# Kernel tuning notes

Hardware: AMD Instinct MI355X
Metric: run time of the kernel (lower is better)

The kernel has to match this reference:

```python
import jax, jax.numpy as jnp
import numpy as np

N = 100_000   # nodes
E = 1_600_000 # edges (avg degree 16)
D = 64        # node feature / conv width
L = 3         # num conv layers
M = 128       # final mlp hidden
BN_EPS = 1e-5


def setup_inputs() -> dict:
    key = jax.random.key(0)
    ks = jax.random.split(key, 12)
    s = np.float32(1.0 / np.sqrt(D))
    sm = np.float32(1.0 / np.sqrt(M))
    return dict(
        x=jax.random.normal(ks[0], (N, D), jnp.float32),
        edge_src=jax.random.randint(ks[1], (E,), 0, N, dtype=jnp.int32),
        edge_dst=jax.random.randint(ks[2], (E,), 0, N, dtype=jnp.int32),
        W1=jax.random.normal(ks[3], (L, D, D), jnp.float32) * s,
        b1=jnp.zeros((L, D), jnp.float32),
        g1=jnp.ones((L, D), jnp.float32),
        be1=jnp.zeros((L, D), jnp.float32),
        W2=jax.random.normal(ks[4], (L, D, D), jnp.float32) * s,
        b2=jnp.zeros((L, D), jnp.float32),
        eps_gin=jnp.zeros((L,), jnp.float32),  # train_eps=True, init 0
        g_bn=jnp.ones((L, D), jnp.float32),
        b_bn=jnp.zeros((L, D), jnp.float32),
        Wf1=jax.random.normal(ks[5], (D, M), jnp.float32) * s,
        bf1=jnp.zeros((M,), jnp.float32),
        gf=jnp.ones((M,), jnp.float32),
        bef=jnp.zeros((M,), jnp.float32),
        Wf2=jax.random.normal(ks[6], (M, 1), jnp.float32) * sm,
        bf2=jnp.zeros((1,), jnp.float32),
    )


def _bn(h, g, b):
    # BatchNorm1d training-mode forward over node dim (biased variance)
    m = h.mean(axis=0)
    v = h.var(axis=0)
    return (h - m) * jax.lax.rsqrt(v + BN_EPS) * g + b


def reference(x, edge_src, edge_dst, W1, b1, g1, be1, W2, b2, eps_gin,
              g_bn, b_bn, Wf1, bf1, gf, bef, Wf2, bf2):
    for i in range(L):
        # GIN aggregation: sum of neighbor features (scatter-add over edges)
        agg = jax.ops.segment_sum(x[edge_src], edge_dst, num_segments=N)
        h = (1.0 + eps_gin[i]) * x + agg
        # GIN nn: Linear -> BatchNorm -> LeakyReLU -> Linear
        h = h @ W1[i] + b1[i]
        h = jax.nn.leaky_relu(_bn(h, g1[i], be1[i]))  # slope 0.01 = torch default
        x = h @ W2[i] + b2[i]
        # outer BatchNorm + activation on all but last conv layer
        if i != L - 1:
            x = jax.nn.leaky_relu(_bn(x, g_bn[i], b_bn[i]))
    # final head: Linear -> BN -> LeakyReLU -> Linear(->1), flatten
    h = x @ Wf1 + bf1
    h = jax.nn.leaky_relu(_bn(h, gf, bef))
    out = h @ Wf2 + bf2
    return out.ravel()  # [N]
```

## Files before the change

kernel.cpp:

```cpp
#include <hip/hip_runtime.h>

#define LRELU(x) ((x) > 0.0f ? (x) : 0.01f * (x))
#define UAF __uint_as_float
#define NSLOT 16

#if defined(__has_builtin)
#if __has_builtin(__builtin_amdgcn_fdot2_f32_bf16)
#define HAS_DOT2BF 1
#endif
#endif
#ifndef HAS_DOT2BF
#define HAS_DOT2BF 0
#endif

__device__ inline uint pack_bf16_rne(float x, float y) {
    uint lo = __float_as_uint(x);
    uint hi = __float_as_uint(y);
    lo = (lo + 0x7fffu + ((lo >> 16) & 1u)) >> 16;
    hi = (hi + 0x7fffu + ((hi >> 16) & 1u)) & 0xffff0000u;
    return lo | hi;
}

__device__ inline float dot2bf(uint a, uint b, float c) {
#if HAS_DOT2BF
    typedef __bf16 bf16x2 __attribute__((ext_vector_type(2)));
    return __builtin_amdgcn_fdot2_f32_bf16(__builtin_bit_cast(bf16x2, a),
                                           __builtin_bit_cast(bf16x2, b), c, false);
#else
    c += UAF(a << 16) * UAF(b << 16);
    c += UAF(a & 0xffff0000u) * UAF(b & 0xffff0000u);
    return c;
#endif
}

__global__ void zero_kernel(float* p, int n) {
    int i = blockIdx.x * blockDim.x + threadIdx.x;
    if (i < n) p[i] = 0.0f;
}

__global__ __launch_bounds__(256) void bhist_kernel(const int* __restrict__ dst,
                                                    int* __restrict__ bcnt, int E, int NB) {
    __shared__ int h[512];
    for (int i = threadIdx.x; i < NB; i += 256) h[i] = 0;
    __syncthreads();
    int base = blockIdx.x * 8192;
    int end = min(E, base + 8192);
    for (int e = base + threadIdx.x; e < end; e += 256) atomicAdd(&h[dst[e] >> 8], 1);
    __syncthreads();
    for (int i = threadIdx.x; i < NB; i += 256)
        if (h[i]) atomicAdd(&bcnt[i], h[i]);
}

__global__ __launch_bounds__(512) void bscan_kernel(const int* __restrict__ bcnt,
                                                    int* __restrict__ boff,
                                                    int* __restrict__ bcur, int NB) {
    __shared__ int sh[512];
    int t = threadIdx.x;
    int v = (t < NB) ? bcnt[t] : 0;
    sh[t] = v;
    __syncthreads();
    for (int o = 1; o < 512; o <<= 1) {
        int u = (t >= o) ? sh[t - o] : 0;
        __syncthreads();
        sh[t] += u;
        __syncthreads();
    }
    if (t < NB) {
        boff[t] = sh[t] - v;
        bcur[t] = sh[t] - v;
    }
}

__global__ __launch_bounds__(256) void bscatter_kernel(const int* __restrict__ src,
                                                       const int* __restrict__ dst,
                                                       int* __restrict__ bcur,
                                                       uint* __restrict__ pairs, int E, int NB) {
    __shared__ int h[512];
    __shared__ int bbase[512];
    for (int i = threadIdx.x; i < NB; i += 256) h[i] = 0;
    __syncthreads();
    int base = blockIdx.x * 8192;
    int end = min(E, base + 8192);
    for (int e = base + threadIdx.x; e < end; e += 256) atomicAdd(&h[dst[e] >> 8], 1);
    __syncthreads();
    for (int i = threadIdx.x; i < NB; i += 256) {
        bbase[i] = h[i] ? atomicAdd(&bcur[i], h[i]) : 0;
        h[i] = 0;
    }
    __syncthreads();
    for (int e = base + threadIdx.x; e < end; e += 256) {
        int d = dst[e];
        int b = d >> 8;
        int o = atomicAdd(&h[b], 1);
        pairs[bbase[b] + o] = ((uint)src[e] << 8) | (uint)(d & 255);
    }
}

__global__ __launch_bounds__(256) void bcsr_kernel(const uint* __restrict__ pairs,
                                                   const int* __restrict__ boff,
                                                   int* __restrict__ ptr, int* __restrict__ cnt,
                                                   int* __restrict__ nbr, int N, int NB, int E) {
    __shared__ int h[256];
    __shared__ int sc[256];
    int b = blockIdx.x;
    int lo = boff[b];
    int hi = (b + 1 < NB) ? boff[b + 1] : E;
    int t = threadIdx.x;
    h[t] = 0;
    __syncthreads();
    for (int i = lo + t; i < hi; i += 256) atomicAdd(&h[pairs[i] & 255u], 1);
    __syncthreads();
    int v = h[t];
    sc[t] = v;
    __syncthreads();
    for (int o = 1; o < 256; o <<= 1) {
        int u = (t >= o) ? sc[t - o] : 0;
        __syncthreads();
        sc[t] += u;
        __syncthreads();
    }
    int excl = sc[t] - v;
    int node = (b << 8) + t;
    if (node < N) {
        ptr[node] = lo + excl;
        cnt[node] = v;
    }
    __syncthreads();
    h[t] = excl;
    __syncthreads();
    for (int i = lo + t; i < hi; i += 256) {
        uint p = pairs[i];
        int ld = p & 255u;
        int o = atomicAdd(&h[ld], 1);
        nbr[lo + o] = (int)(p >> 8);
    }
}

__global__ void packw_kernel(const float* __restrict__ W1, const float* __restrict__ W2,
                             uint* __restrict__ Wp) {
    int id = blockIdx.x * blockDim.x + threadIdx.x;
    if (id >= 6 * 2048) return;
    int mat = id >> 11;
    int r = id & 2047;
    int kp = r >> 6, c = r & 63;
    const float* Ws = (mat < 3) ? (W1 + (size_t)mat * 4096) : (W2 + (size_t)(mat - 3) * 4096);
    Wp[id] = pack_bf16_rne(Ws[(size_t)(2 * kp) * 64 + c], Ws[(size_t)(2 * kp + 1) * 64 + c]);
}

__global__ __launch_bounds__(256) void to_bf16_kernel(const float* __restrict__ in,
                                                      uint* __restrict__ table, int n8) {
    int i = blockIdx.x * blockDim.x + threadIdx.x;
    if (i >= n8) return;
    float4 a = *(const float4*)&in[(size_t)i * 8];
    float4 b = *(const float4*)&in[(size_t)i * 8 + 4];
    uint4 p = make_uint4(pack_bf16_rne(a.x, a.y), pack_bf16_rne(a.z, a.w),
                         pack_bf16_rne(b.x, b.y), pack_bf16_rne(b.z, b.w));
    *(uint4*)&table[(size_t)i * 4] = p;
}

__global__ void finalize_kernel(const float* __restrict__ sums, const float* __restrict__ g,
                                const float* __restrict__ be, float* __restrict__ scale,
                                float* __restrict__ shift, int C, float invN) {
    int d = threadIdx.x;
    if (d >= C) return;
    float s = 0.0f, s2 = 0.0f;
    for (int k = 0; k < NSLOT; k++) {
        s += sums[k * 2 * C + d];
        s2 += sums[k * 2 * C + C + d];
    }
    float mean = s * invN;
    float var = s2 * invN - mean * mean;
    float sc = g[d] * rsqrtf(var + 1e-5f);
    scale[d] = sc;
    shift[d] = be[d] - mean * sc;
}

template <bool ACT>
__global__ __launch_bounds__(256) void gather_kernel(
    const uint* __restrict__ tb, const int* __restrict__ ptr, const int* __restrict__ cnt,
    const int* __restrict__ nbr, const float* __restrict__ eps_gin, int layer,
    const float* __restrict__ scale, const float* __restrict__ shift, uint* __restrict__ agg,
    int N) {
    int gtid = blockIdx.x * blockDim.x + threadIdx.x;
    int node = gtid >> 6;
    if (node >= N) return;
    int lane = threadIdx.x & 63;
    int half = lane >> 5;
    int sl = lane & 31;
    float sc0 = 1.0f, sh0 = 0.0f, sc1 = 1.0f, sh1 = 0.0f;
    if (ACT) {
        sc0 = scale[2 * sl + 0];
        sh0 = shift[2 * sl + 0];
        sc1 = scale[2 * sl + 1];
        sh1 = shift[2 * sl + 1];
    }
    int start = ptr[node];
    int deg = cnt[node];
    float a0 = 0.0f, a1 = 0.0f;
    int j = half;
    for (; j + 14 < deg; j += 16) {
        int ni[8];
        uint vv[8];
#pragma unroll
        for (int q = 0; q < 8; q++) ni[q] = nbr[start + j + 2 * q];
#pragma unroll
        for (int q = 0; q < 8; q++) vv[q] = tb[(size_t)ni[q] * 32 + sl];
#pragma unroll
        for (int q = 0; q < 8; q++) {
            float f0 = UAF(vv[q] << 16), f1 = UAF(vv[q] & 0xffff0000u);
            if (ACT) {
                f0 = LRELU(f0 * sc0 + sh0);
                f1 = LRELU(f1 * sc1 + sh1);
            }
            a0 += f0;
            a1 += f1;
        }
    }
    for (; j + 6 < deg; j += 8) {
        int ni[4];
        uint vv[4];
#pragma unroll
        for (int q = 0; q < 4; q++) ni[q] = nbr[start + j + 2 * q];
#pragma unroll
        for (int q = 0; q < 4; q++) vv[q] = tb[(size_t)ni[q] * 32 + sl];
#pragma unroll
        for (int q = 0; q < 4; q++) {
            float f0 = UAF(vv[q] << 16), f1 = UAF(vv[q] & 0xffff0000u);
            if (ACT) {
                f0 = LRELU(f0 * sc0 + sh0);
                f1 = LRELU(f1 * sc1 + sh1);
            }
            a0 += f0;
            a1 += f1;
        }
    }
    for (; j < deg; j += 2) {
        uint vA = tb[(size_t)nbr[start + j] * 32 + sl];
        float f0 = UAF(vA << 16), f1 = UAF(vA & 0xffff0000u);
        if (ACT) {
            f0 = LRELU(f0 * sc0 + sh0);
            f1 = LRELU(f1 * sc1 + sh1);
        }
        a0 += f0;
        a1 += f1;
    }
    a0 += __shfl(a0, lane ^ 32);
    a1 += __shfl(a1, lane ^ 32);
    uint vs = tb[(size_t)node * 32 + sl];
    float s0 = UAF(vs << 16), s1 = UAF(vs & 0xffff0000u);
    if (ACT) {
        s0 = LRELU(s0 * sc0 + sh0);
        s1 = LRELU(s1 * sc1 + sh1);
    }
    float ep = 1.0f + eps_gin[layer];
    a0 += ep * s0;
    a1 += ep * s1;
    if (half == 0) agg[(size_t)node * 32 + sl] = pack_bf16_rne(a0, a1);
}

template <bool INBN, bool OUTB, int MINW>
__global__ __launch_bounds__(256, MINW) void gemm_bf16_kernel(
    const uint* __restrict__ inb, const float* __restrict__ inf, const uint* __restrict__ Wp,
    const float* __restrict__ bias, const float* __restrict__ scale,
    const float* __restrict__ shift, uint* __restrict__ outb, float* __restrict__ outf,
    float* __restrict__ sums, int nrows) {
    constexpr int COLS = 64;
    __shared__ uint smem[32 * 68 + 32 * COLS];
    uint* inT = smem;
    uint* wsb = smem + 32 * 68;
    int t = threadIdx.x;
    int row0 = blockIdx.x * 64;

    if (!INBN) {
        for (int i = 0; i < 2; i++) {
            int f = t + 256 * i;
            int r = f >> 3, q = f & 7;
            int gr = row0 + r;
            uint4 v = make_uint4(0, 0, 0, 0);
            if (gr < nrows) v = *(const uint4*)&inb[(size_t)gr * 32 + q * 4];
            inT[(4 * q + 0) * 68 + r] = v.x;
            inT[(4 * q + 1) * 68 + r] = v.y;
            inT[(4 * q + 2) * 68 + r] = v.z;
            inT[(4 * q + 3) * 68 + r] = v.w;
        }
    } else {
        for (int i = 0; i < 4; i++) {
            int f = t + 256 * i;
            int r = f >> 4, q = f & 15;
            int gr = row0 + r;
            float4 v = make_float4(0.f, 0.f, 0.f, 0.f);
            if (gr < nrows) v = *(const float4*)&inf[(size_t)gr * 64 + q * 4];
            int d = 4 * q;
            float e0 = LRELU(v.x * scale[d + 0] + shift[d + 0]);
            float e1 = LRELU(v.y * scale[d + 1] + shift[d + 1]);
            float e2 = LRELU(v.z * scale[d + 2] + shift[d + 2]);
            float e3 = LRELU(v.w * scale[d + 3] + shift[d + 3]);
            inT[(2 * q + 0) * 68 + r] = pack_bf16_rne(e0, e1);
            inT[(2 * q + 1) * 68 + r] = pack_bf16_rne(e2, e3);
        }
    }
    for (int i = 0; i < 2; i++) {
        int f = (t + 256 * i) * 4;
        *(uint4*)&wsb[f] = *(const uint4*)&Wp[f];
    }
    __syncthreads();

    int rg = t >> 4, cg = t & 15;
    int r0 = rg * 4, c0 = cg * 4;
    float acc[4][4];
#pragma unroll
    for (int r = 0; r < 4; r++)
#pragma unroll
        for (int c = 0; c < 4; c++) acc[r][c] = 0.0f;

#pragma unroll 8
    for (int kp = 0; kp < 32; kp++) {
        uint4 a = *(const uint4*)&inT[kp * 68 + r0];
        uint av[4] = {a.x, a.y, a.z, a.w};
        uint4 w = *(const uint4*)&wsb[kp * COLS + c0];
        uint wv[4] = {w.x, w.y, w.z, w.w};
#pragma unroll
        for (int r = 0; r < 4; r++)
#pragma unroll
            for (int c = 0; c < 4; c++) acc[r][c] = dot2bf(av[r], wv[c], acc[r][c]);
    }

    float ps[4], ps2[4];
#pragma unroll
    for (int c = 0; c < 4; c++) ps[c] = ps2[c] = 0.0f;
    float4 bv = *(const float4*)&bias[c0];
#pragma unroll
    for (int r = 0; r < 4; r++) {
        int gr = row0 + r0 + r;
        if (gr < nrows) {
            float o0 = acc[r][0] + bv.x;
            float o1 = acc[r][1] + bv.y;
            float o2 = acc[r][2] + bv.z;
            float o3 = acc[r][3] + bv.w;
            if (OUTB) {
                uint2 pk = make_uint2(pack_bf16_rne(o0, o1), pack_bf16_rne(o2, o3));
                *(uint2*)&outb[(size_t)gr * 32 + (c0 >> 1)] = pk;
            } else {
                *(float4*)&outf[(size_t)gr * 64 + c0] = make_float4(o0, o1, o2, o3);
            }
            ps[0] += o0;
            ps2[0] += o0 * o0;
            ps[1] += o1;
            ps2[1] += o1 * o1;
            ps[2] += o2;
            ps2[2] += o2 * o2;
            ps[3] += o3;
            ps2[3] += o3 * o3;
        }
    }

    if (sums == nullptr) return;

    __syncthreads();
    float* red = (float*)smem;
    float* red2 = red + 16 * COLS;
    *(float4*)&red[rg * COLS + c0] = *(float4*)&ps[0];
    *(float4*)&red2[rg * COLS + c0] = *(float4*)&ps2[0];
    __syncthreads();
    if (t < COLS) {
        float s = 0.0f, s2 = 0.0f;
#pragma unroll
        for (int j = 0; j < 16; j++) {
            s += red[j * COLS + t];
            s2 += red2[j * COLS + t];
        }
        int slot = blockIdx.x & (NSLOT - 1);
        atomicAdd(&sums[slot * 2 * COLS + t], s);
        atomicAdd(&sums[slot * 2 * COLS + COLS + t], s2);
    }
}

__global__ __launch_bounds__(256, 4) void gemm_f32_head_kernel(const float* __restrict__ in,
                                                               const float* __restrict__ W,
                                                               const float* __restrict__ bias,
                                                               float* __restrict__ out,
                                                               float* __restrict__ sums,
                                                               int nrows) {
    constexpr int COLS = 128;
    __shared__ float inT[64][68];
    __shared__ float ws[64][COLS];
    int t = threadIdx.x;
    int row0 = blockIdx.x * 64;

    for (int i = 0; i < 4; i++) {
        int f = t + 256 * i;
        int r = f >> 4, ch = f & 15;
        int gr = row0 + r;
        float4 v = make_float4(0.f, 0.f, 0.f, 0.f);
        if (gr < nrows) v = *(const float4*)&in[(size_t)gr * 64 + ch * 4];
        inT[ch * 4 + 0][r] = v.x;
        inT[ch * 4 + 1][r] = v.y;
        inT[ch * 4 + 2][r] = v.z;
        inT[ch * 4 + 3][r] = v.w;
    }
    for (int i = 0; i < COLS / 16; i++) {
        int f = t + 256 * i;
        int k = f / (COLS / 4), c4 = f % (COLS / 4);
        *(float4*)&ws[k][c4 * 4] = *(const float4*)&W[(size_t)k * COLS + c4 * 4];
    }
    __syncthreads();

    int rg = t >> 4, cg = t & 15;
    int r0 = rg * 4, c0 = cg * 4;
    float acc[4][8];
#pragma unroll
    for (int r = 0; r < 4; r++)
#pragma unroll
        for (int c = 0; c < 8; c++) acc[r][c] = 0.0f;

#pragma unroll 16
    for (int k = 0; k < 64; k++) {
        float4 a = *(const float4*)&inT[k][r0];
        float ar[4] = {a.x, a.y, a.z, a.w};
#pragma unroll
        for (int jj = 0; jj < 2; jj++) {
            float4 w4 = *(const float4*)&ws[k][c0 + jj * 64];
            float wr[4] = {w4.x, w4.y, w4.z, w4.w};
#pragma unroll
            for (int r = 0; r < 4; r++)
#pragma unroll
                for (int c = 0; c < 4; c++) acc[r][jj * 4 + c] += ar[r] * wr[c];
        }
    }

    float ps[8], ps2[8];
#pragma unroll
    for (int c = 0; c < 8; c++) ps[c] = ps2[c] = 0.0f;
#pragma unroll
    for (int r = 0; r < 4; r++) {
        int gr = row0 + r0 + r;
        if (gr < nrows) {
#pragma unroll
            for (int jj = 0; jj < 2; jj++) {
                float4 bv = *(const float4*)&bias[c0 + jj * 64];
                float4 o = make_float4(acc[r][jj * 4 + 0] + bv.x, acc[r][jj * 4 + 1] + bv.y,
                                       acc[r][jj * 4 + 2] + bv.z, acc[r][jj * 4 + 3] + bv.w);
                *(float4*)&out[(size_t)gr * COLS + c0 + jj * 64] = o;
                ps[jj * 4 + 0] += o.x;
                ps2[jj * 4 + 0] += o.x * o.x;
                ps[jj * 4 + 1] += o.y;
                ps2[jj * 4 + 1] += o.y * o.y;
                ps[jj * 4 + 2] += o.z;
                ps2[jj * 4 + 2] += o.z * o.z;
                ps[jj * 4 + 3] += o.w;
                ps2[jj * 4 + 3] += o.w * o.w;
            }
        }
    }

    __syncthreads();
    float* red = &inT[0][0];
    float* red2 = red + 16 * COLS;
#pragma unroll
    for (int jj = 0; jj < 2; jj++) {
        *(float4*)&red[rg * COLS + c0 + jj * 64] = *(float4*)&ps[jj * 4];
        *(float4*)&red2[rg * COLS + c0 + jj * 64] = *(float4*)&ps2[jj * 4];
    }
    __syncthreads();
    if (t < COLS) {
        float s = 0.0f, s2 = 0.0f;
#pragma unroll
        for (int j = 0; j < 16; j++) {
            s += red[j * COLS + t];
            s2 += red2[j * COLS + t];
        }
        int slot = blockIdx.x & (NSLOT - 1);
        atomicAdd(&sums[slot * 2 * COLS + t], s);
        atomicAdd(&sums[slot * 2 * COLS + COLS + t], s2);
    }
}

__global__ void head_out_kernel(const float* __restrict__ hf, const float* __restrict__ scale,
                                const float* __restrict__ shift, const float* __restrict__ Wf2,
                                const float* __restrict__ bf2, float* __restrict__ out,
                                int nrows) {
    int gtid = blockIdx.x * blockDim.x + threadIdx.x;
    int wid = gtid >> 6;
    int l = threadIdx.x & 63;
    if (wid >= nrows) return;
    float v0 = hf[(size_t)wid * 128 + l];
    float v1 = hf[(size_t)wid * 128 + 64 + l];
    v0 = LRELU(v0 * scale[l] + shift[l]);
    v1 = LRELU(v1 * scale[64 + l] + shift[64 + l]);
    float p = v0 * Wf2[l] + v1 * Wf2[64 + l];
    for (int o = 32; o > 0; o >>= 1) p += __shfl_down(p, o);
    if (l == 0) out[wid] = p + bf2[0];
}

extern "C" void kernel_launch(void* const* d_in, const int* in_sizes, int n_in, void* d_out,
                              int out_size, void* d_ws, size_t ws_size, hipStream_t stream) {
    const float* x = (const float*)d_in[0];
    const int* esrc = (const int*)d_in[1];
    const int* edst = (const int*)d_in[2];
    const float* W1 = (const float*)d_in[3];
    const float* b1 = (const float*)d_in[4];
    const float* g1 = (const float*)d_in[5];
    const float* be1 = (const float*)d_in[6];
    const float* W2 = (const float*)d_in[7];
    const float* b2 = (const float*)d_in[8];
    const float* eps_gin = (const float*)d_in[9];
    const float* g_bn = (const float*)d_in[10];
    const float* b_bn = (const float*)d_in[11];
    const float* Wf1 = (const float*)d_in[12];
    const float* bf1 = (const float*)d_in[13];
    const float* gf = (const float*)d_in[14];
    const float* bef = (const float*)d_in[15];
    const float* Wf2 = (const float*)d_in[16];
    const float* bf2 = (const float*)d_in[17];
    float* out = (float*)d_out;

    int N = in_sizes[0] / 64;
    int E = in_sizes[1];
    int NB = (N + 255) / 256;
    float invN = 1.0f / (float)N;

    float* ws = (float*)d_ws;
    size_t ND = (size_t)N * 64;
    uint* table = (uint*)ws;
    uint* pairs = (uint*)(ws + ND / 2);
    float* X = ws;
    float* h1 = ws + ND;
    uint* agg = (uint*)(ws + 2 * ND);
    float* HF = ws + ND;
    float* stats = ws + 3 * ND;
    float* ssarea = stats + 5 * NSLOT * 128 + NSLOT * 256;
    int* ibase = (int*)(ssarea + 5 * 128 + 256);
    int* bcnt = ibase;
    int* bcur = ibase + 512;
    int* boff = ibase + 1024;
    int* cnt = ibase + 1536;
    int* ptr = cnt + N;
    int* nbr = ptr + N;
    uint* Wp = (uint*)(nbr + E);

    int nzero = 5 * NSLOT * 128 + NSLOT * 256 + 5 * 128 + 256 + 512;
    zero_kernel<<<(nzero + 255) / 256, 256, 0, stream>>>(stats, nzero);

    int eb = (E + 8191) / 8192;
    bhist_kernel<<<eb, 256, 0, stream>>>(edst, bcnt, E, NB);
    bscan_kernel<<<1, 512, 0, stream>>>(bcnt, boff, bcur, NB);
    bscatter_kernel<<<eb, 256, 0, stream>>>(esrc, edst, bcur, pairs, E, NB);
    bcsr_kernel<<<NB, 256, 0, stream>>>(pairs, boff, ptr, cnt, nbr, N, NB, E);
    packw_kernel<<<(6 * 2048 + 255) / 256, 256, 0, stream>>>(W1, W2, Wp);

    int n8 = N * 8;
    int gg = (N + 63) / 64;
    int gblocks = (N * 64 + 255) / 256;
    to_bf16_kernel<<<(n8 + 255) / 256, 256, 0, stream>>>(x, table, n8);

    for (int i = 0; i < 3; i++) {
        float* st = stats + (size_t)(2 * i) * NSLOT * 128;
        float* so = stats + (size_t)(2 * i + 1) * NSLOT * 128;
        float* st_ss = ssarea + (size_t)(2 * i) * 128;
        float* so_ss = ssarea + (size_t)(2 * i + 1) * 128;
        if (i == 0) {
            gather_kernel<false><<<gblocks, 256, 0, stream>>>(table, ptr, cnt, nbr, eps_gin, i,
                                                              nullptr, nullptr, agg, N);
        } else {
            float* sp_ss = ssarea + (size_t)(2 * (i - 1) + 1) * 128;
            gather_kernel<true><<<gblocks, 256, 0, stream>>>(table, ptr, cnt, nbr, eps_gin, i,
                                                             sp_ss, sp_ss + 64, agg, N);
        }
        gemm_bf16_kernel<false, false, 6><<<gg, 256, 0, stream>>>(
            agg, nullptr, Wp + (size_t)i * 2048, b1 + (size_t)i * 64, nullptr, nullptr, nullptr,
            h1, st, N);
        finalize_kernel<<<1, 64, 0, stream>>>(st, g1 + (size_t)i * 64, be1 + (size_t)i * 64,
                                              st_ss, st_ss + 64, 64, invN);
        if (i < 2) {
            gemm_bf16_kernel<true, true, 6><<<gg, 256, 0, stream>>>(
                nullptr, h1, Wp + (size_t)(3 + i) * 2048, b2 + (size_t)i * 64, st_ss, st_ss + 64,
                table, nullptr, so, N);
            finalize_kernel<<<1, 64, 0, stream>>>(so, g_bn + (size_t)i * 64,
                                                  b_bn + (size_t)i * 64, so_ss, so_ss + 64, 64,
                                                  invN);
        } else {
            gemm_bf16_kernel<true, false, 6><<<gg, 256, 0, stream>>>(
                nullptr, h1, Wp + (size_t)(3 + i) * 2048, b2 + (size_t)i * 64, st_ss, st_ss + 64,
                nullptr, X, nullptr, N);
        }
    }

    float* sf = stats + (size_t)5 * NSLOT * 128;
    float* sf_ss = ssarea + 5 * 128;
    gemm_f32_head_kernel<<<gg, 256, 0, stream>>>(X, Wf1, bf1, HF, sf, N);
    finalize_kernel<<<1, 128, 0, stream>>>(sf, gf, bef, sf_ss, sf_ss + 128, 128, invN);
    head_out_kernel<<<(N + 3) / 4, 256, 0, stream>>>(HF, sf_ss, sf_ss + 128, Wf2, bf2, out, N);
}
```

Measured before the change: 376.5 us.

## Recompute first GEMM instead of storing intermediates; fuse head output into GEMM

The first GEMM per layer now only produces BN statistics and no longer writes the fp32 h1 activation. A second fused kernel recomputes that GEMM from agg, applies BN and LeakyReLU, and runs the second GEMM. The head does the same: one pass gathers statistics, and a second recomputes the 64x128 GEMM and fuses BN, LeakyReLU and the final dot product, so the 128-wide HF buffer is never written or read. This trades extra compute and shared memory for much less global memory traffic.

```diff
diff --git a/kernel.cpp b/kernel.cpp
--- a/kernel.cpp
+++ b/kernel.cpp
@@ -258,46 +258,26 @@
     if (half == 0) agg[(size_t)node * 32 + sl] = pack_bf16_rne(a0, a1);
 }
 
-template <bool INBN, bool OUTB, int MINW>
-__global__ __launch_bounds__(256, MINW) void gemm_bf16_kernel(
-    const uint* __restrict__ inb, const float* __restrict__ inf, const uint* __restrict__ Wp,
-    const float* __restrict__ bias, const float* __restrict__ scale,
-    const float* __restrict__ shift, uint* __restrict__ outb, float* __restrict__ outf,
-    float* __restrict__ sums, int nrows) {
-    constexpr int COLS = 64;
-    __shared__ uint smem[32 * 68 + 32 * COLS];
+__global__ __launch_bounds__(256, 6) void gin_stats_kernel(const uint* __restrict__ inb,
+                                                           const uint* __restrict__ Wp,
+                                                           const float* __restrict__ bias,
+                                                           float* __restrict__ sums, int nrows) {
+    __shared__ uint smem[32 * 68 + 2048];
     uint* inT = smem;
     uint* wsb = smem + 32 * 68;
     int t = threadIdx.x;
     int row0 = blockIdx.x * 64;
 
-    if (!INBN) {
-        for (int i = 0; i < 2; i++) {
-            int f = t + 256 * i;
-            int r = f >> 3, q = f & 7;
-            int gr = row0 + r;
-            uint4 v = make_uint4(0, 0, 0, 0);
-            if (gr < nrows) v = *(const uint4*)&inb[(size_t)gr * 32 + q * 4];
-            inT[(4 * q + 0) * 68 + r] = v.x;
-            inT[(4 * q + 1) * 68 + r] = v.y;
-            inT[(4 * q + 2) * 68 + r] = v.z;
-            inT[(4 * q + 3) * 68 + r] = v.w;
-        }
-    } else {
-        for (int i = 0; i < 4; i++) {
-            int f = t + 256 * i;
-            int r = f >> 4, q = f & 15;
-            int gr = row0 + r;
-            float4 v = make_float4(0.f, 0.f, 0.f, 0.f);
-            if (gr < nrows) v = *(const float4*)&inf[(size_t)gr * 64 + q * 4];
-            int d = 4 * q;
-            float e0 = LRELU(v.x * scale[d + 0] + shift[d + 0]);
-            float e1 = LRELU(v.y * scale[d + 1] + shift[d + 1]);
-            float e2 = LRELU(v.z * scale[d + 2] + shift[d + 2]);
-            float e3 = LRELU(v.w * scale[d + 3] + shift[d + 3]);
-            inT[(2 * q + 0) * 68 + r] = pack_bf16_rne(e0, e1);
-            inT[(2 * q + 1) * 68 + r] = pack_bf16_rne(e2, e3);
-        }
+    for (int i = 0; i < 2; i++) {
+        int f = t + 256 * i;
+        int r = f >> 3, q = f & 7;
+        int gr = row0 + r;
+        uint4 v = make_uint4(0, 0, 0, 0);
+        if (gr < nrows) v = *(const uint4*)&inb[(size_t)gr * 32 + q * 4];
+        inT[(4 * q + 0) * 68 + r] = v.x;
+        inT[(4 * q + 1) * 68 + r] = v.y;
+        inT[(4 * q + 2) * 68 + r] = v.z;
+        inT[(4 * q + 3) * 68 + r] = v.w;
     }
     for (int i = 0; i < 2; i++) {
         int f = (t + 256 * i) * 4;
@@ -317,7 +297,7 @@
     for (int kp = 0; kp < 32; kp++) {
         uint4 a = *(const uint4*)&inT[kp * 68 + r0];
         uint av[4] = {a.x, a.y, a.z, a.w};
-        uint4 w = *(const uint4*)&wsb[kp * COLS + c0];
+        uint4 w = *(const uint4*)&wsb[kp * 64 + c0];
         uint wv[4] = {w.x, w.y, w.z, w.w};
 #pragma unroll
         for (int r = 0; r < 4; r++)
@@ -329,6 +309,135 @@
 #pragma unroll
     for (int c = 0; c < 4; c++) ps[c] = ps2[c] = 0.0f;
     float4 bv = *(const float4*)&bias[c0];
+#pragma unroll
+    for (int r = 0; r < 4; r++) {
+        int gr = row0 + r0 + r;
+        if (gr < nrows) {
+            float o0 = acc[r][0] + bv.x;
+            float o1 = acc[r][1] + bv.y;
+            float o2 = acc[r][2] + bv.z;
+            float o3 = acc[r][3] + bv.w;
+            ps[0] += o0;
+            ps2[0] += o0 * o0;
+            ps[1] += o1;
+            ps2[1] += o1 * o1;
+            ps[2] += o2;
+            ps2[2] += o2 * o2;
+            ps[3] += o3;
+            ps2[3] += o3 * o3;
+        }
+    }
+
+    __syncthreads();
+    float* red = (float*)smem;
+    float* red2 = red + 16 * 64;
+    *(float4*)&red[rg * 64 + c0] = *(float4*)&ps[0];
+    *(float4*)&red2[rg * 64 + c0] = *(float4*)&ps2[0];
+    __syncthreads();
+    if (t < 64) {
+        float s = 0.0f, s2 = 0.0f;
+#pragma unroll
+        for (int j = 0; j < 16; j++) {
+            s += red[j * 64 + t];
+            s2 += red2[j * 64 + t];
+        }
+        int slot = blockIdx.x & (NSLOT - 1);
+        atomicAdd(&sums[slot * 128 + t], s);
+        atomicAdd(&sums[slot * 128 + 64 + t], s2);
+    }
+}
+
+template <bool OUTB>
+__global__ __launch_bounds__(256, 6) void gemm2_kernel(
+    const uint* __restrict__ agg, const uint* __restrict__ W1p, const float* __restrict__ b1,
+    const float* __restrict__ scale, const float* __restrict__ shift,
+    const uint* __restrict__ W2p, const float* __restrict__ b2, uint* __restrict__ outb,
+    float* __restrict__ outf, float* __restrict__ sums, int nrows) {
+    __shared__ uint smem[32 * 68 + 4096];
+    uint* inT = smem;
+    uint* w1 = smem + 32 * 68;
+    uint* w2 = w1 + 2048;
+    int t = threadIdx.x;
+    int row0 = blockIdx.x * 64;
+
+    for (int i = 0; i < 2; i++) {
+        int f = t + 256 * i;
+        int r = f >> 3, q = f & 7;
+        int gr = row0 + r;
+        uint4 v = make_uint4(0, 0, 0, 0);
+        if (gr < nrows) v = *(const uint4*)&agg[(size_t)gr * 32 + q * 4];
+        inT[(4 * q + 0) * 68 + r] = v.x;
+        inT[(4 * q + 1) * 68 + r] = v.y;
+        inT[(4 * q + 2) * 68 + r] = v.z;
+        inT[(4 * q + 3) * 68 + r] = v.w;
+    }
+    for (int i = 0; i < 2; i++) {
+        int f = (t + 256 * i) * 4;
+        *(uint4*)&w1[f] = *(const uint4*)&W1p[f];
+        *(uint4*)&w2[f] = *(const uint4*)&W2p[f];
+    }
+    __syncthreads();
+
+    int rg = t >> 4, cg = t & 15;
+    int r0 = rg * 4, c0 = cg * 4;
+    float acc[4][4];
+#pragma unroll
+    for (int r = 0; r < 4; r++)
+#pragma unroll
+        for (int c = 0; c < 4; c++) acc[r][c] = 0.0f;
+
+#pragma unroll 8
+    for (int kp = 0; kp < 32; kp++) {
+        uint4 a = *(const uint4*)&inT[kp * 68 + r0];
+        uint av[4] = {a.x, a.y, a.z, a.w};
+        uint4 w = *(const uint4*)&w1[kp * 64 + c0];
+        uint wv[4] = {w.x, w.y, w.z, w.w};
+#pragma unroll
+        for (int r = 0; r < 4; r++)
+#pragma unroll
+            for (int c = 0; c < 4; c++) acc[r][c] = dot2bf(av[r], wv[c], acc[r][c]);
+    }
+
+    float4 bv1 = *(const float4*)&b1[c0];
+    float4 scv = *(const float4*)&scale[c0];
+    float4 shv = *(const float4*)&shift[c0];
+    __syncthreads();
+#pragma unroll
+    for (int r = 0; r < 4; r++) {
+        float o0 = acc[r][0] + bv1.x;
+        float o1 = acc[r][1] + bv1.y;
+        float o2 = acc[r][2] + bv1.z;
+        float o3 = acc[r][3] + bv1.w;
+        float e0 = LRELU(o0 * scv.x + shv.x);
+        float e1 = LRELU(o1 * scv.y + shv.y);
+        float e2 = LRELU(o2 * scv.z + shv.z);
+        float e3 = LRELU(o3 * scv.w + shv.w);
+        inT[(c0 >> 1) * 68 + r0 + r] = pack_bf16_rne(e0, e1);
+        inT[((c0 >> 1) + 1) * 68 + r0 + r] = pack_bf16_rne(e2, e3);
+    }
+    __syncthreads();
+
+#pragma unroll
+    for (int r = 0; r < 4; r++)
+#pragma unroll
+        for (int c = 0; c < 4; c++) acc[r][c] = 0.0f;
+
+#pragma unroll 8
+    for (int kp = 0; kp < 32; kp++) {
+        uint4 a = *(const uint4*)&inT[kp * 68 + r0];
+        uint av[4] = {a.x, a.y, a.z, a.w};
+        uint4 w = *(const uint4*)&w2[kp * 64 + c0];
+        uint wv[4] = {w.x, w.y, w.z, w.w};
+#pragma unroll
+        for (int r = 0; r < 4; r++)
+#pragma unroll
+            for (int c = 0; c < 4; c++) acc[r][c] = dot2bf(av[r], wv[c], acc[r][c]);
+    }
+
+    float ps[4], ps2[4];
+#pragma unroll
+    for (int c = 0; c < 4; c++) ps[c] = ps2[c] = 0.0f;
+    float4 bv = *(const float4*)&b2[c0];
 #pragma unroll
     for (int r = 0; r < 4; r++) {
         int gr = row0 + r0 + r;
@@ -358,29 +467,28 @@
 
     __syncthreads();
     float* red = (float*)smem;
-    float* red2 = red + 16 * COLS;
-    *(float4*)&red[rg * COLS + c0] = *(float4*)&ps[0];
-    *(float4*)&red2[rg * COLS + c0] = *(float4*)&ps2[0];
-    __syncthreads();
-    if (t < COLS) {
+    float* red2 = red + 16 * 64;
+    *(float4*)&red[rg * 64 + c0] = *(float4*)&ps[0];
+    *(float4*)&red2[rg * 64 + c0] = *(float4*)&ps2[0];
+    __syncthreads();
+    if (t < 64) {
         float s = 0.0f, s2 = 0.0f;
 #pragma unroll
         for (int j = 0; j < 16; j++) {
-            s += red[j * COLS + t];
-            s2 += red2[j * COLS + t];
+            s += red[j * 64 + t];
+            s2 += red2[j * 64 + t];
         }
         int slot = blockIdx.x & (NSLOT - 1);
-        atomicAdd(&sums[slot * 2 * COLS + t], s);
-        atomicAdd(&sums[slot * 2 * COLS + COLS + t], s2);
-    }
-}
-
-__global__ __launch_bounds__(256, 4) void gemm_f32_head_kernel(const float* __restrict__ in,
-                                                               const float* __restrict__ W,
-                                                               const float* __restrict__ bias,
-                                                               float* __restrict__ out,
-                                                               float* __restrict__ sums,
-                                                               int nrows) {
+        atomicAdd(&sums[slot * 128 + t], s);
+        atomicAdd(&sums[slot * 128 + 64 + t], s2);
+    }
+}
+
+__global__ __launch_bounds__(256, 4) void headstats_kernel(const float* __restrict__ in,
+                                                           const float* __restrict__ W,
+                                                           const float* __restrict__ bias,
+                                                           float* __restrict__ sums,
+                                                           int nrows) {
     constexpr int COLS = 128;
     __shared__ float inT[64][68];
     __shared__ float ws[64][COLS];
@@ -440,7 +548,6 @@
                 float4 bv = *(const float4*)&bias[c0 + jj * 64];
                 float4 o = make_float4(acc[r][jj * 4 + 0] + bv.x, acc[r][jj * 4 + 1] + bv.y,
                                        acc[r][jj * 4 + 2] + bv.z, acc[r][jj * 4 + 3] + bv.w);
-                *(float4*)&out[(size_t)gr * COLS + c0 + jj * 64] = o;
                 ps[jj * 4 + 0] += o.x;
                 ps2[jj * 4 + 0] += o.x * o.x;
                 ps[jj * 4 + 1] += o.y;
@@ -475,21 +582,80 @@
     }
 }
 
-__global__ void head_out_kernel(const float* __restrict__ hf, const float* __restrict__ scale,
-                                const float* __restrict__ shift, const float* __restrict__ Wf2,
-                                const float* __restrict__ bf2, float* __restrict__ out,
-                                int nrows) {
-    int gtid = blockIdx.x * blockDim.x + threadIdx.x;
-    int wid = gtid >> 6;
-    int l = threadIdx.x & 63;
-    if (wid >= nrows) return;
-    float v0 = hf[(size_t)wid * 128 + l];
-    float v1 = hf[(size_t)wid * 128 + 64 + l];
-    v0 = LRELU(v0 * scale[l] + shift[l]);
-    v1 = LRELU(v1 * scale[64 + l] + shift[64 + l]);
-    float p = v0 * Wf2[l] + v1 * Wf2[64 + l];
-    for (int o = 32; o > 0; o >>= 1) p += __shfl_down(p, o);
-    if (l == 0) out[wid] = p + bf2[0];
+__global__ __launch_bounds__(256, 4) void headout_kernel(
+    const float* __restrict__ in, const float* __restrict__ W, const float* __restrict__ bias,
+    const float* __restrict__ scale, const float* __restrict__ shift,
+    const float* __restrict__ Wf2, const float* __restrict__ bf2, float* __restrict__ out,
+    int nrows) {
+    constexpr int COLS = 128;
+    __shared__ float inT[64][68];
+    __shared__ float ws[64][COLS];
+    int t = threadIdx.x;
+    int row0 = blockIdx.x * 64;
+
+    for (int i = 0; i < 4; i++) {
+        int f = t + 256 * i;
+        int r = f >> 4, ch = f & 15;
+        int gr = row0 + r;
+        float4 v = make_float4(0.f, 0.f, 0.f, 0.f);
+        if (gr < nrows) v = *(const float4*)&in[(size_t)gr * 64 + ch * 4];
+        inT[ch * 4 + 0][r] = v.x;
+        inT[ch * 4 + 1][r] = v.y;
+        inT[ch * 4 + 2][r] = v.z;
+        inT[ch * 4 + 3][r] = v.w;
+    }
+    for (int i = 0; i < COLS / 16; i++) {
+        int f = t + 256 * i;
+        int k = f / (COLS / 4), c4 = f % (COLS / 4);
+        *(float4*)&ws[k][c4 * 4] = *(const float4*)&W[(size_t)k * COLS + c4 * 4];
+    }
+    __syncthreads();
+
+    int rg = t >> 4, cg = t & 15;
+    int r0 = rg * 4, c0 = cg * 4;
+    float acc[4][8];
+#pragma unroll
+    for (int r = 0; r < 4; r++)
+#pragma unroll
+        for (int c = 0; c < 8; c++) acc[r][c] = 0.0f;
+
+#pragma unroll 16
+    for (int k = 0; k < 64; k++) {
+        float4 a = *(const float4*)&inT[k][r0];
+        float ar[4] = {a.x, a.y, a.z, a.w};
+#pragma unroll
+        for (int jj = 0; jj < 2; jj++) {
+            float4 w4 = *(const float4*)&ws[k][c0 + jj * 64];
+            float wr[4] = {w4.x, w4.y, w4.z, w4.w};
+#pragma unroll
+            for (int r = 0; r < 4; r++)
+#pragma unroll
+                for (int c = 0; c < 4; c++) acc[r][jj * 4 + c] += ar[r] * wr[c];
+        }
+    }
+
+    float p[4] = {0.f, 0.f, 0.f, 0.f};
+#pragma unroll
+    for (int jj = 0; jj < 2; jj++) {
+        float4 bv = *(const float4*)&bias[c0 + jj * 64];
+        float4 scv = *(const float4*)&scale[c0 + jj * 64];
+        float4 shv = *(const float4*)&shift[c0 + jj * 64];
+        float4 wv = *(const float4*)&Wf2[c0 + jj * 64];
+#pragma unroll
+        for (int r = 0; r < 4; r++) {
+            float e0 = LRELU((acc[r][jj * 4 + 0] + bv.x) * scv.x + shv.x);
+            float e1 = LRELU((acc[r][jj * 4 + 1] + bv.y) * scv.y + shv.y);
+            float e2 = LRELU((acc[r][jj * 4 + 2] + bv.z) * scv.z + shv.z);
+            float e3 = LRELU((acc[r][jj * 4 + 3] + bv.w) * scv.w + shv.w);
+            p[r] += e0 * wv.x + e1 * wv.y + e2 * wv.z + e3 * wv.w;
+        }
+    }
+#pragma unroll
+    for (int r = 0; r < 4; r++) {
+        for (int o = 1; o < 16; o <<= 1) p[r] += __shfl_xor(p[r], o);
+        int gr = row0 + r0 + r;
+        if (cg == 0 && gr < nrows) out[gr] = p[r] + bf2[0];
+    }
 }
 
 extern "C" void kernel_launch(void* const* d_in, const int* in_sizes, int n_in, void* d_out,
@@ -524,9 +690,7 @@
     uint* table = (uint*)ws;
     uint* pairs = (uint*)(ws + ND / 2);
     float* X = ws;
-    float* h1 = ws + ND;
     uint* agg = (uint*)(ws + 2 * ND);
-    float* HF = ws + ND;
     float* stats = ws + 3 * ND;
     float* ssarea = stats + 5 * NSLOT * 128 + NSLOT * 256;
     int* ibase = (int*)(ssarea + 5 * 128 + 256);
@@ -566,28 +730,27 @@
             gather_kernel<true><<<gblocks, 256, 0, stream>>>(table, ptr, cnt, nbr, eps_gin, i,
                                                              sp_ss, sp_ss + 64, agg, N);
         }
-        gemm_bf16_kernel<false, false, 6><<<gg, 256, 0, stream>>>(
-            agg, nullptr, Wp + (size_t)i * 2048, b1 + (size_t)i * 64, nullptr, nullptr, nullptr,
-            h1, st, N);
+        gin_stats_kernel<<<gg, 256, 0, stream>>>(agg, Wp + (size_t)i * 2048,
+                                                 b1 + (size_t)i * 64, st, N);
         finalize_kernel<<<1, 64, 0, stream>>>(st, g1 + (size_t)i * 64, be1 + (size_t)i * 64,
                                               st_ss, st_ss + 64, 64, invN);
         if (i < 2) {
-            gemm_bf16_kernel<true, true, 6><<<gg, 256, 0, stream>>>(
-                nullptr, h1, Wp + (size_t)(3 + i) * 2048, b2 + (size_t)i * 64, st_ss, st_ss + 64,
-                table, nullptr, so, N);
+            gemm2_kernel<true><<<gg, 256, 0, stream>>>(
+                agg, Wp + (size_t)i * 2048, b1 + (size_t)i * 64, st_ss, st_ss + 64,
+                Wp + (size_t)(3 + i) * 2048, b2 + (size_t)i * 64, table, nullptr, so, N);
             finalize_kernel<<<1, 64, 0, stream>>>(so, g_bn + (size_t)i * 64,
                                                   b_bn + (size_t)i * 64, so_ss, so_ss + 64, 64,
                                                   invN);
         } else {
-            gemm_bf16_kernel<true, false, 6><<<gg, 256, 0, stream>>>(
-                nullptr, h1, Wp + (size_t)(3 + i) * 2048, b2 + (size_t)i * 64, st_ss, st_ss + 64,
-                nullptr, X, nullptr, N);
+            gemm2_kernel<false><<<gg, 256, 0, stream>>>(
+                agg, Wp + (size_t)i * 2048, b1 + (size_t)i * 64, st_ss, st_ss + 64,
+                Wp + (size_t)(3 + i) * 2048, b2 + (size_t)i * 64, nullptr, X, nullptr, N);
         }
     }
 
     float* sf = stats + (size_t)5 * NSLOT * 128;
     float* sf_ss = ssarea + 5 * 128;
-    gemm_f32_head_kernel<<<gg, 256, 0, stream>>>(X, Wf1, bf1, HF, sf, N);
+    headstats_kernel<<<gg, 256, 0, stream>>>(X, Wf1, bf1, sf, N);
     finalize_kernel<<<1, 128, 0, stream>>>(sf, gf, bef, sf_ss, sf_ss + 128, 128, invN);
-    head_out_kernel<<<(N + 3) / 4, 256, 0, stream>>>(HF, sf_ss, sf_ss + 128, Wf2, bf2, out, N);
-}
+    headout_kernel<<<gg, 256, 0, stream>>>(X, Wf1, bf1, sf_ss, sf_ss + 128, Wf2, bf2, out, N);
+}
```

New measurement: 404.7 us. 7.5% more time.
